# Optimization experiments

Hardware: AMD Instinct MI355X
Metric: run time of the kernel (lower is better)

Reference implementation:

```python
import jax, jax.numpy as jnp
import numpy as np
from jax import lax

K = 31          # mip_kernel
P_LO, P_HI = 0.01, 0.99
ALPHA = 0.15
MU = 10.0
PD_ITERS = 30
TAU = 0.125
SIG = 0.125
THETA = 1.0
EPS = 1e-6


def _max_pool(x, k):
    # torch F.max_pool2d with stride=1, padding=k//2 pads with -inf
    p = k // 2
    return lax.reduce_window(
        x, -jnp.inf, lax.max,
        window_dimensions=(1, 1, k, k),
        window_strides=(1, 1, 1, 1),
        padding=[(0, 0), (0, 0), (p, p), (p, p)])


def _forward_grad(u):
    # forward differences, zero-padded on the far edge (same shape as u)
    dx = jnp.pad(u[..., :, 1:] - u[..., :, :-1], ((0, 0), (0, 0), (0, 0), (0, 1)))
    dy = jnp.pad(u[..., 1:, :] - u[..., :-1, :], ((0, 0), (0, 0), (0, 1), (0, 0)))
    return dx, dy


def _divergence(px, py):
    div_x = px - jnp.pad(px[..., :, :-1], ((0, 0), (0, 0), (0, 0), (1, 0)))
    div_y = py - jnp.pad(py[..., :-1, :], ((0, 0), (0, 0), (1, 0), (0, 0)))
    return div_x + div_y


def _robust_normalize(x):
    B = x.shape[0]
    flat = x.reshape(B, -1)
    lo = jnp.quantile(flat, P_LO, axis=1).reshape(B, 1, 1, 1)
    hi = jnp.quantile(flat, P_HI, axis=1).reshape(B, 1, 1, 1)
    return jnp.clip((x - lo) / (hi - lo + EPS), 0.0, 1.0)


def setup_inputs() -> dict:
    key = jax.random.key(0)
    Iy = jax.random.uniform(key, (16, 3, 512, 512), dtype=jnp.float32)
    return {"Iy": Iy}


def reference(Iy):
    B = Iy.shape[0]
    R, G, Bc = Iy[:, 0:1], Iy[:, 1:2], Iy[:, 2:3]

    Rmax = _max_pool(R, K)
    GBmax = jnp.maximum(_max_pool(G, K), _max_pool(Bc, K))
    Dmip_abs = jnp.abs(Rmax - GBmax)

    N_hat = _robust_normalize(Dmip_abs + R)

    dxh, dyh = _forward_grad(N_hat)
    grad_mag = jnp.sqrt(dxh * dxh + dyh * dyh + EPS)
    # sigma_mode == 'median' -> per-image median of grad magnitude
    sigma = jnp.quantile(grad_mag.reshape(B, -1), 0.5, axis=1).reshape(B, 1, 1, 1)
    sigma = jnp.maximum(sigma, EPS)

    Wx = 1.0 + MU * jnp.exp(-jnp.abs(dxh) / sigma)
    Wy = 1.0 + MU * jnp.exp(-jnp.abs(dyh) / sigma)

    def step(carry, _):
        u, u_bar, px, py = carry
        dx, dy = _forward_grad(u_bar)
        px = jnp.clip(px + SIG * dx, -ALPHA * Wx, ALPHA * Wx)
        py = jnp.clip(py + SIG * dy, -ALPHA * Wy, ALPHA * Wy)
        div_p = _divergence(px, py)
        v = u + TAU * div_p
        u_new = (v + TAU * N_hat) / (1.0 + TAU)
        u_bar = u_new + THETA * (u_new - u)
        return (u_new, u_bar, px, py), None

    z = jnp.zeros_like(N_hat)
    (u, _, _, _), _ = lax.scan(step, (N_hat, N_hat, z, z), None, length=PD_ITERS)
    return jnp.clip(u, 0.0, 1.0)
```

## Files before the change

kernel.cpp:

```cpp
#include <hip/hip_runtime.h>
#include <hip/hip_bf16.h>
#include <hip/hip_fp16.h>
#include <math.h>

#define NPIX   262144
#define NP     4194304
#define NBINS  8192
#define HSUB   16
#define RB     8
#define SIG    0.125f
#define TAUC   0.125f
#define ALPHAC 0.15f
#define MUC    10.0f
#define EPSC   1e-6f
#define NEGINF -3.4e38f
#define IVT    (1.0f / (1.0f + TAUC))

__device__ __forceinline__ void cvt8h(float4 raw, float* d) {
    const __half2* h = (const __half2*)&raw;
#pragma unroll
    for (int j = 0; j < 4; ++j) {
        float2 f = __half22float2(h[j]);
        d[2 * j] = f.x; d[2 * j + 1] = f.y;
    }
}
__device__ __forceinline__ void ld8h(const __half* p, float* d) {
    cvt8h(*(const float4*)p, d);
}
__device__ __forceinline__ void ld8f(const float* p, float* d) {
    float4 t0 = *(const float4*)p;
    float4 t1 = *(const float4*)(p + 4);
    d[0]=t0.x; d[1]=t0.y; d[2]=t0.z; d[3]=t0.w;
    d[4]=t1.x; d[5]=t1.y; d[6]=t1.z; d[7]=t1.w;
}
__device__ __forceinline__ float4 pk8h(const float* s) {
    float4 r; __half2* h = (__half2*)&r;
#pragma unroll
    for (int j = 0; j < 4; ++j) h[j] = __floats2half2_rn(s[2 * j], s[2 * j + 1]);
    return r;
}
__device__ __forceinline__ float bnd(float d, float inv) {
    return ALPHAC * (1.f + MUC * __expf(-fabsf(d) * inv));
}
__device__ __forceinline__ float clmp(float v, float b) {
    return fminf(fmaxf(v, -b), b);
}


__global__ __launch_bounds__(512) void hpass3_k(const float* __restrict__ Iy,
                                                float* __restrict__ H) {
    __shared__ float rowbuf[8][512];
    __shared__ float PB[8][512];
    __shared__ float SB[8][512];
    int tid = threadIdx.x;
    int plane = blockIdx.y;
    int y0 = blockIdx.x * 8;

#pragma unroll
    for (int q = 0; q < 2; ++q) {
        int idx = q * 512 + tid;
        int r = idx >> 7;
        int x4 = (idx & 127) << 2;
        float4 v;
        if (plane < 16) {
            v = *(const float4*)(Iy + (size_t)(plane * 3) * NPIX + (size_t)(y0 + r) * 512 + x4);
        } else {
            int b = plane - 16;
            float4 g = *(const float4*)(Iy + ((size_t)(b * 3) + 1) * NPIX + (size_t)(y0 + r) * 512 + x4);
            float4 bb = *(const float4*)(Iy + ((size_t)(b * 3) + 2) * NPIX + (size_t)(y0 + r) * 512 + x4);
            v = make_float4(fmaxf(g.x, bb.x), fmaxf(g.y, bb.y), fmaxf(g.z, bb.z), fmaxf(g.w, bb.w));
        }
        *(float4*)(&rowbuf[r][x4]) = v;
    }
    __syncthreads();

    if (tid < 272) {
        int type = tid / 136;
        int rem = tid % 136;
        int r = rem / 17;
        int seg = rem % 17;
        int s0 = seg * 31;
        if (type == 0) {
            float run = rowbuf[r][s0];
            PB[r][s0] = run;
            for (int j = 1; j < 31; ++j) {
                int idx = s0 + j;
                if (idx < 512) { run = fmaxf(run, rowbuf[r][idx]); PB[r][idx] = run; }
            }
        } else {
            int s1 = min(s0 + 30, 511);
            float run = rowbuf[r][s1];
            SB[r][s1] = run;
            for (int j = s1 - 1; j >= s0; --j) { run = fmaxf(run, rowbuf[r][j]); SB[r][j] = run; }
        }
    }
    __syncthreads();

    int x = tid, a = x - 15, bc = x + 15;
#pragma unroll
    for (int r = 0; r < 8; ++r) {
        float o;
        if (a < 0)        o = PB[r][bc];
        else if (bc > 511) o = fmaxf(SB[r][a], PB[r][511]);
        else              o = fmaxf(SB[r][a], PB[r][bc]);
        H[(size_t)plane * NPIX + (size_t)(y0 + r) * 512 + x] = o;
    }
}

__global__ __launch_bounds__(64) void vpassC_k(const float* __restrict__ H,
                                               const float* __restrict__ Iy,
                                               float* __restrict__ xb) {
    int x = blockIdx.x * 64 + threadIdx.x;
    int b = blockIdx.z;
    const float* inR = H + (size_t)b * NPIX;
    const float* inM = H + (size_t)(16 + b) * NPIX;
    const float* IyR = Iy + (size_t)(b * 3) * NPIX;
    float*       out = xb + (size_t)b * NPIX;
    int c0 = blockIdx.y * 2;

    float SprevR[31], SprevM[31];
    if (c0 > 0) {
        int s0 = (c0 - 1) * 31;
        float vR[31], vM[31];
#pragma unroll
        for (int j = 0; j < 31; ++j) {
            vR[j] = inR[(size_t)(s0 + j) * 512 + x];
            vM[j] = inM[(size_t)(s0 + j) * 512 + x];
        }
        float aR = NEGINF, aM = NEGINF;
#pragma unroll
        for (int j = 30; j >= 0; --j) {
            aR = fmaxf(aR, vR[j]); SprevR[j] = aR;
            aM = fmaxf(aM, vM[j]); SprevM[j] = aM;
        }
    } else {
#pragma unroll
        for (int j = 0; j < 31; ++j) { SprevR[j] = NEGINF; SprevM[j] = NEGINF; }
    }

    int send = min(c0 + 1, 16);
    for (int s = c0; s <= send; ++s) {
        int s0 = s * 31;
        float vR[31], vM[31];
#pragma unroll
        for (int j = 0; j < 31; ++j) {
            bool ok = (s0 + j < 512);
            vR[j] = ok ? inR[(size_t)(s0 + j) * 512 + x] : NEGINF;
            vM[j] = ok ? inM[(size_t)(s0 + j) * 512 + x] : NEGINF;
        }
        float ScurR[31], ScurM[31];
        float aR = NEGINF, aM = NEGINF;
#pragma unroll
        for (int j = 30; j >= 0; --j) {
            aR = fmaxf(aR, vR[j]); ScurR[j] = aR;
            aM = fmaxf(aM, vM[j]); ScurM[j] = aM;
        }
        float PR = NEGINF, PM = NEGINF;
#pragma unroll
        for (int r = 0; r < 31; ++r) {
            PR = fmaxf(PR, vR[r]);
            PM = fmaxf(PM, vM[r]);
            int i = s0 + r - 15;
            if (i >= 0 && i <= 511) {
                int a = s0 - 30 + r;
                float oR, oM;
                if (a < 0) { oR = PR; oM = PM; }
                else {
                    float SvR = (r == 30) ? ScurR[0] : SprevR[r + 1];
                    float SvM = (r == 30) ? ScurM[0] : SprevM[r + 1];
                    oR = fmaxf(SvR, PR);
                    oM = fmaxf(SvM, PM);
                }
                out[(size_t)i * 512 + x] = fabsf(oR - oM) + IyR[(size_t)i * 512 + x];
            }
        }
#pragma unroll
        for (int j = 0; j < 31; ++j) { SprevR[j] = ScurR[j]; SprevM[j] = ScurM[j]; }
    }
}


__global__ __launch_bounds__(1024) void zeroi_k(int* __restrict__ p) {
    p[blockIdx.x * 1024 + threadIdx.x] = 0;
}

__global__ __launch_bounds__(1024) void hist2_k(const float* __restrict__ v,
                                                int* __restrict__ hist) {
    __shared__ int lh[NBINS];
    int s = blockIdx.x, b = blockIdx.y, tid = threadIdx.x;
    for (int i = tid; i < NBINS; i += 1024) lh[i] = 0;
    __syncthreads();
    const float* p = v + (size_t)b * NPIX + (size_t)s * (NPIX / HSUB);
    for (int i = tid; i < NPIX / HSUB; i += 1024) {
        int bin = (int)(p[i] * (NBINS * 0.5f));
        bin = min(max(bin, 0), NBINS - 1);
        atomicAdd(&lh[bin], 1);
    }
    __syncthreads();
    for (int i = tid; i < NBINS; i += 1024) {
        int c = lh[i];
        if (c) atomicAdd(&hist[b * NBINS + i], c);
    }
}

__global__ __launch_bounds__(1024) void gradhisth_k(const __half* __restrict__ nh,
                                                    int* __restrict__ hist) {
    __shared__ int lh[NBINS];
    int s = blockIdx.x, b = blockIdx.y, tid = threadIdx.x;
    for (int i = tid; i < NBINS; i += 1024) lh[i] = 0;
    __syncthreads();
    const __half* p = nh + (size_t)b * NPIX;
    int base = s * (NPIX / HSUB);
    for (int ii = tid; ii < NPIX / HSUB; ii += 1024) {
        int i = base + ii;
        float c = __half2float(p[i]);
        int x = i & 511, y = i >> 9;
        float dx = (x < 511) ? __half2float(p[i + 1])   - c : 0.f;
        float dy = (y < 511) ? __half2float(p[i + 512]) - c : 0.f;
        float gm = sqrtf(dx * dx + dy * dy + EPSC);
        int bin = (int)(gm * (NBINS * 0.5f));
        bin = min(max(bin, 0), NBINS - 1);
        atomicAdd(&lh[bin], 1);
    }
    __syncthreads();
    for (int i = tid; i < NBINS; i += 1024) {
        int c = lh[i];
        if (c) atomicAdd(&hist[b * NBINS + i], c);
    }
}

__global__ __launch_bounds__(1024) void quant2_k(const int* __restrict__ hist,
                                                 float* __restrict__ scal,
                                                 float q0, float q1, int s0, int s1) {
    __shared__ int csum[1025];
    __shared__ int wsum[16];
    int b = blockIdx.x, tid = threadIdx.x;
    const int* h = hist + b * NBINS;
    int s = 0;
#pragma unroll
    for (int j = 0; j < NBINS / 1024; ++j) s += h[tid * (NBINS / 1024) + j];

    int lane = tid & 63, wave = tid >> 6;
    int v = s;
#pragma unroll
    for (int off = 1; off < 64; off <<= 1) {
        int n = __shfl_up(v, off, 64);
        if (lane >= off) v += n;
    }
    if (lane == 63) wsum[wave] = v;
    __syncthreads();
    if (wave == 0 && lane < 16) {
        int w = wsum[lane];
#pragma unroll
        for (int off = 1; off < 16; off <<= 1) {
            int n = __shfl_up(w, off, 64);
            if (lane >= off) w += n;
        }
        wsum[lane] = w;
    }
    __syncthreads();
    int incl = v + (wave > 0 ? wsum[wave - 1] : 0);
    csum[tid + 1] = incl;
    if (tid == 0) csum[0] = 0;
    __syncthreads();

#pragma unroll
    for (int pass = 0; pass < 2; ++pass) {
        int slot = pass ? s1 : s0;
        if (slot < 0) continue;
        float q = pass ? q1 : q0;
        float t = q * (float)(NPIX - 1);
        if ((float)csum[tid] <= t && (float)csum[tid + 1] > t) {
            const int per = NBINS / 1024;
            int cb = csum[tid];
            int bin = tid * per;
            int hv = 1;
            for (int j = 0; j < per; ++j) {
                hv = h[tid * per + j];
                if ((float)(cb + hv) > t) { bin = tid * per + j; break; }
                cb += hv;
            }
            float k = t - (float)cb;
            scal[b * 4 + slot] = ((float)bin + (k + 0.5f) / (float)hv) * (2.0f / NBINS);
        }
    }
}

__global__ __launch_bounds__(256) void nhat2h_k(const float* __restrict__ xb,
                                                const float* __restrict__ scal,
                                                __half* __restrict__ nhh) {
    size_t i = ((size_t)blockIdx.x * 256 + threadIdx.x) * 4;
    int b = (int)(i >> 18);
    float lo = scal[b * 4 + 0], hi = scal[b * 4 + 1];
    float inv = 1.0f / (hi - lo + EPSC);
    float4 v = *(const float4*)(xb + i);
    float a0 = fminf(fmaxf((v.x - lo) * inv, 0.f), 1.f);
    float a1 = fminf(fmaxf((v.y - lo) * inv, 0.f), 1.f);
    float a2 = fminf(fmaxf((v.z - lo) * inv, 0.f), 1.f);
    float a3 = fminf(fmaxf((v.w - lo) * inv, 0.f), 1.f);
    *(__half2*)(nhh + i)     = __floats2half2_rn(a0, a1);
    *(__half2*)(nhh + i + 2) = __floats2half2_rn(a2, a3);
}

__global__ __launch_bounds__(256) void pdf2_k(const __half* __restrict__ u,
                                              const __half* __restrict__ up,
                                              const __half* __restrict__ pxO,
                                              const __half* __restrict__ pyO,
                                              __half* __restrict__ pxN,
                                              __half* __restrict__ pyN,
                                              const __half* __restrict__ nh,
                                              const float* __restrict__ scal,
                                              __half* __restrict__ u1g,
                                              __half* __restrict__ u2g,
                                              float* __restrict__ outF,
                                              int last) {
    __shared__ __align__(16) char smem[75776];
    float  (*ubar0)[512] = (float (*)[512])smem;
    __half (*u1l)[512]   = (__half(*)[512])smem;
    __half (*u0l)[512]   = (__half(*)[512])(smem + 10240);
    __half (*nhl)[512]   = (__half(*)[512])(smem + 24576);
    __half (*px1)[512]   = (__half(*)[512])(smem + 36864);
    __half (*py1)[512]   = (__half(*)[512])(smem + 47104);
    __half (*px2l)[512]  = (__half(*)[512])(smem + 58368);
    __half (*py2l)[512]  = (__half(*)[512])(smem + 66560);

    int tid = threadIdx.x;
    int sub = tid >> 6, lane = tid & 63, x0 = lane * 8;
    int y0 = blockIdx.x * RB;
    int b = blockIdx.y;
    size_t plane = (size_t)b * NPIX;
    float sgm = fmaxf(scal[b * 4 + 2], EPSC);
    float inv = 1.0f / sgm;
    const float4 z4 = make_float4(0.f, 0.f, 0.f, 0.f);

    for (int i = sub; i < 12; i += 4) {
        int g = y0 - 2 + i;
        if (g >= 0 && g < 512) {
            size_t off = plane + (size_t)g * 512 + x0;
            float uu[8], pp[8];
            ld8h(u + off, uu); ld8h(up + off, pp);
#pragma unroll
            for (int j = 0; j < 8; ++j) ubar0[i][x0 + j] = 2.f * uu[j] - pp[j];
            *(float4*)&nhl[i][x0] = *(const float4*)(nh + off);
        } else {
            *(float4*)&ubar0[i][x0]     = z4;
            *(float4*)&ubar0[i][x0 + 4] = z4;
            *(float4*)&nhl[i][x0] = z4;
        }
    }
    __syncthreads();

    for (int c = sub; c < 11; c += 4) {
        int g = y0 - 2 + c;
        if (g >= 0 && g < 512) {
            size_t off = plane + (size_t)g * 512 + x0;
            float nhc[8], nhd[8], ubc[8], ubd[8];
            ld8h(&nhl[c][x0], nhc);
            ld8h(&nhl[c + 1][x0], nhd);
            ld8f(&ubar0[c][x0], ubc);
            ld8f(&ubar0[c + 1][x0], ubd);
            float nhRr = (lane < 63) ? __half2float(nhl[c][x0 + 8]) : 0.f;
            float ubRr = (lane < 63) ? ubar0[c][x0 + 8] : 0.f;
            bool rD = (g < 511);
            float py0v[8]; ld8h(pyO + off, py0v);
            float pyv[8];
#pragma unroll
            for (int j = 0; j < 8; ++j) {
                float by = bnd(rD ? (nhd[j] - nhc[j]) : 0.f, inv);
                float dy = rD ? (ubd[j] - ubc[j]) : 0.f;
                pyv[j] = clmp(py0v[j] + SIG * dy, by);
            }
            *(float4*)&py1[c][x0] = pk8h(pyv);
            if (c >= 1) {
                float px0v[8]; ld8h(pxO + off, px0v);
                float pxv[8];
#pragma unroll
                for (int j = 0; j < 8; ++j) {
                    int x = x0 + j;
                    bool xok = (x < 511);
                    float nhr = (j < 7) ? nhc[j + 1] : nhRr;
                    float ubr = (j < 7) ? ubc[j + 1] : ubRr;
                    float bx = bnd(xok ? (nhr - nhc[j]) : 0.f, inv);
                    float dx = xok ? (ubr - ubc[j]) : 0.f;
                    pxv[j] = clmp(px0v[j] + SIG * dx, bx);
                }
                *(float4*)&px1[c - 1][x0] = pk8h(pxv);
            }
        } else {
            *(float4*)&py1[c][x0] = z4;
            if (c >= 1) *(float4*)&px1[c - 1][x0] = z4;
        }
    }
    __syncthreads();

    for (int a = sub; a < 10; a += 4) {
        int g = y0 - 1 + a;
        if (g >= 0 && g < 512) {
            size_t off = plane + (size_t)g * 512 + x0;
            float4 u0raw = *(const float4*)(u + off);
            float u0v[8]; cvt8h(u0raw, u0v);
            float nhc[8];  ld8h(&nhl[a + 1][x0], nhc);
            float px1c[8]; ld8h(&px1[a][x0], px1c);
            float py1c[8]; ld8h(&py1[a + 1][x0], py1c);
            float py1u[8]; ld8h(&py1[a][x0], py1u);
            float pxl = (x0 > 0) ? __half2float(px1[a][x0 - 1]) : 0.f;
            bool gU = (g > 0);
            float uv[8];
#pragma unroll
            for (int j = 0; j < 8; ++j) {
                int x = x0 + j;
                float left = (x > 0) ? ((j > 0) ? px1c[j - 1] : pxl) : 0.f;
                float div = px1c[j] - left + py1c[j] - (gU ? py1u[j] : 0.f);
                uv[j] = (u0v[j] + TAUC * div + TAUC * nhc[j]) * IVT;
            }
            float4 packed = pk8h(uv);
            *(float4*)&u1l[a][x0] = packed;
            *(float4*)&u0l[a][x0] = u0raw;
            if (g >= y0 && g < y0 + RB) *(float4*)(u1g + off) = packed;
        } else {
            *(float4*)&u1l[a][x0] = z4;
            *(float4*)&u0l[a][x0] = z4;
        }
    }
    __syncthreads();

    for (int e = sub; e < 9; e += 4) {
        int g = y0 - 1 + e;
        if (g >= 0) {
            size_t off = plane + (size_t)g * 512 + x0;
            float u1c[8], u0c[8], u1d[8], u0d[8];
            ld8h(&u1l[e][x0], u1c);     ld8h(&u0l[e][x0], u0c);
            ld8h(&u1l[e + 1][x0], u1d); ld8h(&u0l[e + 1][x0], u0d);
            float nhc[8], nhd[8];
            ld8h(&nhl[e + 1][x0], nhc); ld8h(&nhl[e + 2][x0], nhd);
            float ubc[8], ubd[8];
#pragma unroll
            for (int j = 0; j < 8; ++j) {
                ubc[j] = 2.f * u1c[j] - u0c[j];
                ubd[j] = 2.f * u1d[j] - u0d[j];
            }
            float ubRr = (lane < 63) ? (2.f * __half2float(u1l[e][x0 + 8]) - __half2float(u0l[e][x0 + 8])) : 0.f;
            float nhRr = (lane < 63) ? __half2float(nhl[e + 1][x0 + 8]) : 0.f;
            bool rD = (g < 511);
            float py1c[8]; ld8h(&py1[e + 1][x0], py1c);
            float pyv[8];
#pragma unroll
            for (int j = 0; j < 8; ++j) {
                float by = bnd(rD ? (nhd[j] - nhc[j]) : 0.f, inv);
                float dy = rD ? (ubd[j] - ubc[j]) : 0.f;
                pyv[j] = clmp(py1c[j] + SIG * dy, by);
            }
            float4 pyp = pk8h(pyv);
            *(float4*)&py2l[e][x0] = pyp;
            if (g >= y0) *(float4*)(pyN + off) = pyp;
            if (e >= 1) {
                float px1c[8]; ld8h(&px1[e][x0], px1c);
                float pxv[8];
#pragma unroll
                for (int j = 0; j < 8; ++j) {
                    int x = x0 + j;
                    bool xok = (x < 511);
                    float nhr = (j < 7) ? nhc[j + 1] : nhRr;
                    float ubr = (j < 7) ? ubc[j + 1] : ubRr;
                    float bx = bnd(xok ? (nhr - nhc[j]) : 0.f, inv);
                    float dx = xok ? (ubr - ubc[j]) : 0.f;
                    pxv[j] = clmp(px1c[j] + SIG * dx, bx);
                }
                float4 pxp = pk8h(pxv);
                *(float4*)&px2l[e - 1][x0] = pxp;
                *(float4*)(pxN + off) = pxp;
            }
        } else {
            *(float4*)&py2l[e][x0] = z4;
        }
    }
    __syncthreads();

    for (int d = sub; d < 8; d += 4) {
        int g = y0 + d;
        size_t off = plane + (size_t)g * 512 + x0;
        float px2c[8]; ld8h(&px2l[d][x0], px2c);
        float py2c[8]; ld8h(&py2l[d + 1][x0], py2c);
        float py2u[8]; ld8h(&py2l[d][x0], py2u);
        float pxl = (x0 > 0) ? __half2float(px2l[d][x0 - 1]) : 0.f;
        float u1c[8]; ld8h(&u1l[d + 1][x0], u1c);
        float nhc[8]; ld8h(&nhl[d + 2][x0], nhc);
        bool gU = (g > 0);
        float uv[8];
#pragma unroll
        for (int j = 0; j < 8; ++j) {
            int x = x0 + j;
            float left = (x > 0) ? ((j > 0) ? px2c[j - 1] : pxl) : 0.f;
            float div = px2c[j] - left + py2c[j] - (gU ? py2u[j] : 0.f);
            uv[j] = (u1c[j] + TAUC * div + TAUC * nhc[j]) * IVT;
        }
        if (last) {
            float4 o0, o1;
            o0.x = fminf(fmaxf(uv[0], 0.f), 1.f);
            o0.y = fminf(fmaxf(uv[1], 0.f), 1.f);
            o0.z = fminf(fmaxf(uv[2], 0.f), 1.f);
            o0.w = fminf(fmaxf(uv[3], 0.f), 1.f);
            o1.x = fminf(fmaxf(uv[4], 0.f), 1.f);
            o1.y = fminf(fmaxf(uv[5], 0.f), 1.f);
            o1.z = fminf(fmaxf(uv[6], 0.f), 1.f);
            o1.w = fminf(fmaxf(uv[7], 0.f), 1.f);
            *(float4*)(outF + off)     = o0;
            *(float4*)(outF + off + 4) = o1;
        } else {
            *(float4*)(u2g + off) = pk8h(uv);
        }
    }
}

extern "C" void kernel_launch(void* const* d_in, const int* in_sizes, int n_in,
                              void* d_out, int out_size, void* d_ws, size_t ws_size,
                              hipStream_t stream) {
    const float* Iy = (const float*)d_in[0];
    float* ws = (float*)d_ws;
    float* out = (float*)d_out;

    dim3 hist_g(HSUB, 16);
    dim3 pd2_g(512 / RB, 16);

    float*  xb = ws;
    float*  H  = ws + (size_t)NP;
    __half* hb = (__half*)(ws + (size_t)3 * NP);
    __half* nhh = hb;
    __half* HA  = hb + (size_t)NP;
    __half* HB  = hb + (size_t)2 * NP;
    __half* HC  = hb + (size_t)3 * NP;
    __half* HD  = hb + (size_t)4 * NP;
    __half* pxA = hb + (size_t)5 * NP;
    __half* pyA = hb + (size_t)6 * NP;
    __half* pxB = hb + (size_t)7 * NP;
    __half* pyB = hb + (size_t)8 * NP;
    int*    hist = (int*)(ws + (size_t)15 * NP / 2);
    float*  scal = ws + (size_t)15 * NP / 2 + 16 * NBINS;

    hpass3_k<<<dim3(64, 32), dim3(512), 0, stream>>>(Iy, H);
    vpassC_k<<<dim3(8, 9, 16), dim3(64), 0, stream>>>(H, Iy, xb);

    zeroi_k<<<16 * NBINS / 1024, 1024, 0, stream>>>(hist);
    hist2_k<<<hist_g, 1024, 0, stream>>>(xb, hist);
    quant2_k<<<16, 1024, 0, stream>>>(hist, scal, 0.01f, 0.99f, 0, 1);
    nhat2h_k<<<NP / 1024, 256, 0, stream>>>(xb, scal, nhh);

    zeroi_k<<<16 * NBINS / 1024, 1024, 0, stream>>>(hist);
    gradhisth_k<<<hist_g, 1024, 0, stream>>>(nhh, hist);
    quant2_k<<<16, 1024, 0, stream>>>(hist, scal, 0.5f, 0.5f, 2, -1);
    hipMemsetAsync(pxA, 0, (size_t)2 * NP * sizeof(__half), stream);

    const __half* ucur = nhh;
    const __half* uprev = nhh;
    __half* pxs[2] = {pxA, pxB};
    __half* pys[2] = {pyA, pyB};
    for (int k = 0; k < 15; ++k) {
        int cur = k & 1;
        __half* u1o = (k & 1) ? HC : HA;
        __half* u2o = (k & 1) ? HD : HB;
        pdf2_k<<<pd2_g, 256, 0, stream>>>(ucur, uprev,
                                          pxs[cur], pys[cur],
                                          pxs[cur ^ 1], pys[cur ^ 1],
                                          nhh, scal, u1o, u2o, out,
                                          (k == 14) ? 1 : 0);
        uprev = u1o;
        ucur = u2o;
    }
}
```

Measured before the change: 490.4 us.

## Shrink pdf2 LDS footprint by storing ubar in half and re-reading u/p from global

Cuts the fused two-iteration primal-dual kernel's shared memory from about 74KB to 46KB. It stores the initial ubar in fp16 instead of fp32 and drops the u0, px2 and py2 LDS tiles, re-reading u and the freshly written pxN/pyN from global memory (likely L2 hits). The u1 rows are stashed in registers so they can overwrite the aliased ubar region after an extra barrier. The aim is higher occupancy, at the cost of more global traffic, an extra sync, more registers and fp16 rounding of ubar.

```diff
diff --git a/kernel.cpp b/kernel.cpp
--- a/kernel.cpp
+++ b/kernel.cpp
@@ -26,12 +26,6 @@
 }
 __device__ __forceinline__ void ld8h(const __half* p, float* d) {
     cvt8h(*(const float4*)p, d);
-}
-__device__ __forceinline__ void ld8f(const float* p, float* d) {
-    float4 t0 = *(const float4*)p;
-    float4 t1 = *(const float4*)(p + 4);
-    d[0]=t0.x; d[1]=t0.y; d[2]=t0.z; d[3]=t0.w;
-    d[4]=t1.x; d[5]=t1.y; d[6]=t1.z; d[7]=t1.w;
 }
 __device__ __forceinline__ float4 pk8h(const float* s) {
     float4 r; __half2* h = (__half2*)&r;
@@ -314,15 +308,13 @@
                                               __half* __restrict__ u2g,
                                               float* __restrict__ outF,
                                               int last) {
-    __shared__ __align__(16) char smem[75776];
-    float  (*ubar0)[512] = (float (*)[512])smem;
-    __half (*u1l)[512]   = (__half(*)[512])smem;
-    __half (*u0l)[512]   = (__half(*)[512])(smem + 10240);
-    __half (*nhl)[512]   = (__half(*)[512])(smem + 24576);
-    __half (*px1)[512]   = (__half(*)[512])(smem + 36864);
-    __half (*py1)[512]   = (__half(*)[512])(smem + 47104);
-    __half (*px2l)[512]  = (__half(*)[512])(smem + 58368);
-    __half (*py2l)[512]  = (__half(*)[512])(smem + 66560);
+    __shared__ __align__(16) char smem[47104];
+    __half (*ubar0h)[512] = (__half(*)[512])smem;
+    __half (*u1l)[512]    = (__half(*)[512])smem;
+    __half (*nhl)[512]    = (__half(*)[512])(smem + 12288);
+    __half (*px1)[512]    = (__half(*)[512])(smem + 24576);
+    __half (*py1)[512]    = (__half(*)[512])(smem + 34816);
+    __half*  py2h         = (__half*)(smem + 46080);
 
     int tid = threadIdx.x;
     int sub = tid >> 6, lane = tid & 63, x0 = lane * 8;
@@ -337,14 +329,14 @@
         int g = y0 - 2 + i;
         if (g >= 0 && g < 512) {
             size_t off = plane + (size_t)g * 512 + x0;
-            float uu[8], pp[8];
+            float uu[8], pp[8], ub[8];
             ld8h(u + off, uu); ld8h(up + off, pp);
 #pragma unroll
-            for (int j = 0; j < 8; ++j) ubar0[i][x0 + j] = 2.f * uu[j] - pp[j];
+            for (int j = 0; j < 8; ++j) ub[j] = 2.f * uu[j] - pp[j];
+            *(float4*)&ubar0h[i][x0] = pk8h(ub);
             *(float4*)&nhl[i][x0] = *(const float4*)(nh + off);
         } else {
-            *(float4*)&ubar0[i][x0]     = z4;
-            *(float4*)&ubar0[i][x0 + 4] = z4;
+            *(float4*)&ubar0h[i][x0] = z4;
             *(float4*)&nhl[i][x0] = z4;
         }
     }
@@ -357,10 +349,10 @@
             float nhc[8], nhd[8], ubc[8], ubd[8];
             ld8h(&nhl[c][x0], nhc);
             ld8h(&nhl[c + 1][x0], nhd);
-            ld8f(&ubar0[c][x0], ubc);
-            ld8f(&ubar0[c + 1][x0], ubd);
+            ld8h(&ubar0h[c][x0], ubc);
+            ld8h(&ubar0h[c + 1][x0], ubd);
             float nhRr = (lane < 63) ? __half2float(nhl[c][x0 + 8]) : 0.f;
-            float ubRr = (lane < 63) ? ubar0[c][x0 + 8] : 0.f;
+            float ubRr = (lane < 63) ? __half2float(ubar0h[c][x0 + 8]) : 0.f;
             bool rD = (g < 511);
             float py0v[8]; ld8h(pyO + off, py0v);
             float pyv[8];
@@ -393,19 +385,20 @@
     }
     __syncthreads();
 
+    float u1stash[3][8];
+    int   u1rows = 0;
     for (int a = sub; a < 10; a += 4) {
         int g = y0 - 1 + a;
+        float uv[8];
         if (g >= 0 && g < 512) {
             size_t off = plane + (size_t)g * 512 + x0;
-            float4 u0raw = *(const float4*)(u + off);
-            float u0v[8]; cvt8h(u0raw, u0v);
+            float u0v[8]; ld8h(u + off, u0v);
             float nhc[8];  ld8h(&nhl[a + 1][x0], nhc);
             float px1c[8]; ld8h(&px1[a][x0], px1c);
             float py1c[8]; ld8h(&py1[a + 1][x0], py1c);
             float py1u[8]; ld8h(&py1[a][x0], py1u);
             float pxl = (x0 > 0) ? __half2float(px1[a][x0 - 1]) : 0.f;
             bool gU = (g > 0);
-            float uv[8];
 #pragma unroll
             for (int j = 0; j < 8; ++j) {
                 int x = x0 + j;
@@ -413,13 +406,25 @@
                 float div = px1c[j] - left + py1c[j] - (gU ? py1u[j] : 0.f);
                 uv[j] = (u0v[j] + TAUC * div + TAUC * nhc[j]) * IVT;
             }
-            float4 packed = pk8h(uv);
+        } else {
+#pragma unroll
+            for (int j = 0; j < 8; ++j) uv[j] = 0.f;
+        }
+#pragma unroll
+        for (int j = 0; j < 8; ++j) u1stash[u1rows][j] = uv[j];
+        ++u1rows;
+    }
+    __syncthreads();
+    {
+        int k = 0;
+        for (int a = sub; a < 10; a += 4, ++k) {
+            int g = y0 - 1 + a;
+            float4 packed = pk8h(u1stash[k]);
             *(float4*)&u1l[a][x0] = packed;
-            *(float4*)&u0l[a][x0] = u0raw;
-            if (g >= y0 && g < y0 + RB) *(float4*)(u1g + off) = packed;
-        } else {
-            *(float4*)&u1l[a][x0] = z4;
-            *(float4*)&u0l[a][x0] = z4;
+            if (g >= y0 && g < y0 + RB) {
+                size_t off = plane + (size_t)g * 512 + x0;
+                *(float4*)(u1g + off) = packed;
+            }
         }
     }
     __syncthreads();
@@ -428,20 +433,26 @@
         int g = y0 - 1 + e;
         if (g >= 0) {
             size_t off = plane + (size_t)g * 512 + x0;
-            float u1c[8], u0c[8], u1d[8], u0d[8];
-            ld8h(&u1l[e][x0], u1c);     ld8h(&u0l[e][x0], u0c);
-            ld8h(&u1l[e + 1][x0], u1d); ld8h(&u0l[e + 1][x0], u0d);
+            bool rD = (g < 511);
+            float u1c[8], u1d[8], u0c[8], u0d[8];
+            ld8h(&u1l[e][x0], u1c);
+            ld8h(&u1l[e + 1][x0], u1d);
+            ld8h(u + off, u0c);
+            if (rD) ld8h(u + off + 512, u0d);
+            else {
+#pragma unroll
+                for (int j = 0; j < 8; ++j) u0d[j] = 0.f;
+            }
             float nhc[8], nhd[8];
             ld8h(&nhl[e + 1][x0], nhc); ld8h(&nhl[e + 2][x0], nhd);
             float ubc[8], ubd[8];
 #pragma unroll
             for (int j = 0; j < 8; ++j) {
                 ubc[j] = 2.f * u1c[j] - u0c[j];
-                ubd[j] = 2.f * u1d[j] - u0d[j];
-            }
-            float ubRr = (lane < 63) ? (2.f * __half2float(u1l[e][x0 + 8]) - __half2float(u0l[e][x0 + 8])) : 0.f;
+                ubd[j] = rD ? (2.f * u1d[j] - u0d[j]) : 0.f;
+            }
+            float ubRr = (lane < 63) ? (2.f * __half2float(u1l[e][x0 + 8]) - __half2float(u[off + 8])) : 0.f;
             float nhRr = (lane < 63) ? __half2float(nhl[e + 1][x0 + 8]) : 0.f;
-            bool rD = (g < 511);
             float py1c[8]; ld8h(&py1[e + 1][x0], py1c);
             float pyv[8];
 #pragma unroll
@@ -451,8 +462,8 @@
                 pyv[j] = clmp(py1c[j] + SIG * dy, by);
             }
             float4 pyp = pk8h(pyv);
-            *(float4*)&py2l[e][x0] = pyp;
-            if (g >= y0) *(float4*)(pyN + off) = pyp;
+            if (e == 0) *(float4*)&py2h[x0] = pyp;
+            else        *(float4*)(pyN + off) = pyp;
             if (e >= 1) {
                 float px1c[8]; ld8h(&px1[e][x0], px1c);
                 float pxv[8];
@@ -466,12 +477,10 @@
                     float dx = xok ? (ubr - ubc[j]) : 0.f;
                     pxv[j] = clmp(px1c[j] + SIG * dx, bx);
                 }
-                float4 pxp = pk8h(pxv);
-                *(float4*)&px2l[e - 1][x0] = pxp;
-                *(float4*)(pxN + off) = pxp;
-            }
-        } else {
-            *(float4*)&py2l[e][x0] = z4;
+                *(float4*)(pxN + off) = pk8h(pxv);
+            }
+        } else {
+            *(float4*)&py2h[x0] = z4;
         }
     }
     __syncthreads();
@@ -479,10 +488,12 @@
     for (int d = sub; d < 8; d += 4) {
         int g = y0 + d;
         size_t off = plane + (size_t)g * 512 + x0;
-        float px2c[8]; ld8h(&px2l[d][x0], px2c);
-        float py2c[8]; ld8h(&py2l[d + 1][x0], py2c);
-        float py2u[8]; ld8h(&py2l[d][x0], py2u);
-        float pxl = (x0 > 0) ? __half2float(px2l[d][x0 - 1]) : 0.f;
+        float px2c[8]; ld8h(pxN + off, px2c);
+        float py2c[8]; ld8h(pyN + off, py2c);
+        float py2u[8];
+        if (d == 0) ld8h(&py2h[x0], py2u);
+        else        ld8h(pyN + off - 512, py2u);
+        float pxl = (x0 > 0) ? __half2float(*(pxN + off - 1)) : 0.f;
         float u1c[8]; ld8h(&u1l[d + 1][x0], u1c);
         float nhc[8]; ld8h(&nhl[d + 2][x0], nhc);
         bool gU = (g > 0);
```

Result: slower. 530.7 us (+8.2%).

## Store max-pool intermediates in fp16 and skip final-iteration dual writes

Applied to the files above, without the earlier changes.

The horizontal max-pool output and the pre-normalisation buffer are now stored as fp16 instead of fp32. This halves traffic through hpass, vpass, the histogram and the normalise kernels, and the normalise kernel now handles 8 elements per thread. The last primal-dual iteration no longer writes px, py or u1 to global memory, since nothing reads them afterwards. Histogram zeroing is switched to hipMemsetAsync. Storing the intermediates in fp16 adds rounding before the quantile and clamp steps.

```diff
diff --git a/kernel.cpp b/kernel.cpp
--- a/kernel.cpp
+++ b/kernel.cpp
@@ -27,12 +27,6 @@
 __device__ __forceinline__ void ld8h(const __half* p, float* d) {
     cvt8h(*(const float4*)p, d);
 }
-__device__ __forceinline__ void ld8f(const float* p, float* d) {
-    float4 t0 = *(const float4*)p;
-    float4 t1 = *(const float4*)(p + 4);
-    d[0]=t0.x; d[1]=t0.y; d[2]=t0.z; d[3]=t0.w;
-    d[4]=t1.x; d[5]=t1.y; d[6]=t1.z; d[7]=t1.w;
-}
 __device__ __forceinline__ float4 pk8h(const float* s) {
     float4 r; __half2* h = (__half2*)&r;
 #pragma unroll
@@ -48,7 +42,7 @@
 
 
 __global__ __launch_bounds__(512) void hpass3_k(const float* __restrict__ Iy,
-                                                float* __restrict__ H) {
+                                                __half* __restrict__ H) {
     __shared__ float rowbuf[8][512];
     __shared__ float PB[8][512];
     __shared__ float SB[8][512];
@@ -103,19 +97,19 @@
         if (a < 0)        o = PB[r][bc];
         else if (bc > 511) o = fmaxf(SB[r][a], PB[r][511]);
         else              o = fmaxf(SB[r][a], PB[r][bc]);
-        H[(size_t)plane * NPIX + (size_t)(y0 + r) * 512 + x] = o;
-    }
-}
-
-__global__ __launch_bounds__(64) void vpassC_k(const float* __restrict__ H,
+        H[(size_t)plane * NPIX + (size_t)(y0 + r) * 512 + x] = __float2half_rn(o);
+    }
+}
+
+__global__ __launch_bounds__(64) void vpassC_k(const __half* __restrict__ H,
                                                const float* __restrict__ Iy,
-                                               float* __restrict__ xb) {
+                                               __half* __restrict__ xb) {
     int x = blockIdx.x * 64 + threadIdx.x;
     int b = blockIdx.z;
-    const float* inR = H + (size_t)b * NPIX;
-    const float* inM = H + (size_t)(16 + b) * NPIX;
+    const __half* inR = H + (size_t)b * NPIX;
+    const __half* inM = H + (size_t)(16 + b) * NPIX;
     const float* IyR = Iy + (size_t)(b * 3) * NPIX;
-    float*       out = xb + (size_t)b * NPIX;
+    __half*      out = xb + (size_t)b * NPIX;
     int c0 = blockIdx.y * 2;
 
     float SprevR[31], SprevM[31];
@@ -124,8 +118,8 @@
         float vR[31], vM[31];
 #pragma unroll
         for (int j = 0; j < 31; ++j) {
-            vR[j] = inR[(size_t)(s0 + j) * 512 + x];
-            vM[j] = inM[(size_t)(s0 + j) * 512 + x];
+            vR[j] = __half2float(inR[(size_t)(s0 + j) * 512 + x]);
+            vM[j] = __half2float(inM[(size_t)(s0 + j) * 512 + x]);
         }
         float aR = NEGINF, aM = NEGINF;
 #pragma unroll
@@ -145,8 +139,8 @@
 #pragma unroll
         for (int j = 0; j < 31; ++j) {
             bool ok = (s0 + j < 512);
-            vR[j] = ok ? inR[(size_t)(s0 + j) * 512 + x] : NEGINF;
-            vM[j] = ok ? inM[(size_t)(s0 + j) * 512 + x] : NEGINF;
+            vR[j] = ok ? __half2float(inR[(size_t)(s0 + j) * 512 + x]) : NEGINF;
+            vM[j] = ok ? __half2float(inM[(size_t)(s0 + j) * 512 + x]) : NEGINF;
         }
         float ScurR[31], ScurM[31];
         float aR = NEGINF, aM = NEGINF;
@@ -171,7 +165,8 @@
                     oR = fmaxf(SvR, PR);
                     oM = fmaxf(SvM, PM);
                 }
-                out[(size_t)i * 512 + x] = fabsf(oR - oM) + IyR[(size_t)i * 512 + x];
+                out[(size_t)i * 512 + x] =
+                    __float2half_rn(fabsf(oR - oM) + IyR[(size_t)i * 512 + x]);
             }
         }
 #pragma unroll
@@ -180,19 +175,15 @@
 }
 
 
-__global__ __launch_bounds__(1024) void zeroi_k(int* __restrict__ p) {
-    p[blockIdx.x * 1024 + threadIdx.x] = 0;
-}
-
-__global__ __launch_bounds__(1024) void hist2_k(const float* __restrict__ v,
+__global__ __launch_bounds__(1024) void hist2_k(const __half* __restrict__ v,
                                                 int* __restrict__ hist) {
     __shared__ int lh[NBINS];
     int s = blockIdx.x, b = blockIdx.y, tid = threadIdx.x;
     for (int i = tid; i < NBINS; i += 1024) lh[i] = 0;
     __syncthreads();
-    const float* p = v + (size_t)b * NPIX + (size_t)s * (NPIX / HSUB);
+    const __half* p = v + (size_t)b * NPIX + (size_t)s * (NPIX / HSUB);
     for (int i = tid; i < NPIX / HSUB; i += 1024) {
-        int bin = (int)(p[i] * (NBINS * 0.5f));
+        int bin = (int)(__half2float(p[i]) * (NBINS * 0.5f));
         bin = min(max(bin, 0), NBINS - 1);
         atomicAdd(&lh[bin], 1);
     }
@@ -286,20 +277,19 @@
     }
 }
 
-__global__ __launch_bounds__(256) void nhat2h_k(const float* __restrict__ xb,
+__global__ __launch_bounds__(256) void nhat2h_k(const __half* __restrict__ xb,
                                                 const float* __restrict__ scal,
                                                 __half* __restrict__ nhh) {
-    size_t i = ((size_t)blockIdx.x * 256 + threadIdx.x) * 4;
+    size_t i = ((size_t)blockIdx.x * 256 + threadIdx.x) * 8;
     int b = (int)(i >> 18);
     float lo = scal[b * 4 + 0], hi = scal[b * 4 + 1];
     float inv = 1.0f / (hi - lo + EPSC);
-    float4 v = *(const float4*)(xb + i);
-    float a0 = fminf(fmaxf((v.x - lo) * inv, 0.f), 1.f);
-    float a1 = fminf(fmaxf((v.y - lo) * inv, 0.f), 1.f);
-    float a2 = fminf(fmaxf((v.z - lo) * inv, 0.f), 1.f);
-    float a3 = fminf(fmaxf((v.w - lo) * inv, 0.f), 1.f);
-    *(__half2*)(nhh + i)     = __floats2half2_rn(a0, a1);
-    *(__half2*)(nhh + i + 2) = __floats2half2_rn(a2, a3);
+    float v[8]; ld8h(xb + i, v);
+    float a[8];
+#pragma unroll
+    for (int j = 0; j < 8; ++j)
+        a[j] = fminf(fmaxf((v[j] - lo) * inv, 0.f), 1.f);
+    *(float4*)(nhh + i) = pk8h(a);
 }
 
 __global__ __launch_bounds__(256) void pdf2_k(const __half* __restrict__ u,
@@ -357,8 +347,17 @@
             float nhc[8], nhd[8], ubc[8], ubd[8];
             ld8h(&nhl[c][x0], nhc);
             ld8h(&nhl[c + 1][x0], nhd);
-            ld8f(&ubar0[c][x0], ubc);
-            ld8f(&ubar0[c + 1][x0], ubd);
+            float t0[8], t1[8];
+            float4 a0 = *(float4*)&ubar0[c][x0];
+            float4 a1 = *(float4*)&ubar0[c][x0 + 4];
+            t0[0]=a0.x; t0[1]=a0.y; t0[2]=a0.z; t0[3]=a0.w;
+            t0[4]=a1.x; t0[5]=a1.y; t0[6]=a1.z; t0[7]=a1.w;
+            float4 b0 = *(float4*)&ubar0[c + 1][x0];
+            float4 b1 = *(float4*)&ubar0[c + 1][x0 + 4];
+            t1[0]=b0.x; t1[1]=b0.y; t1[2]=b0.z; t1[3]=b0.w;
+            t1[4]=b1.x; t1[5]=b1.y; t1[6]=b1.z; t1[7]=b1.w;
+#pragma unroll
+            for (int j = 0; j < 8; ++j) { ubc[j] = t0[j]; ubd[j] = t1[j]; }
             float nhRr = (lane < 63) ? __half2float(nhl[c][x0 + 8]) : 0.f;
             float ubRr = (lane < 63) ? ubar0[c][x0 + 8] : 0.f;
             bool rD = (g < 511);
@@ -416,7 +415,7 @@
             float4 packed = pk8h(uv);
             *(float4*)&u1l[a][x0] = packed;
             *(float4*)&u0l[a][x0] = u0raw;
-            if (g >= y0 && g < y0 + RB) *(float4*)(u1g + off) = packed;
+            if (!last && g >= y0 && g < y0 + RB) *(float4*)(u1g + off) = packed;
         } else {
             *(float4*)&u1l[a][x0] = z4;
             *(float4*)&u0l[a][x0] = z4;
@@ -452,7 +451,7 @@
             }
             float4 pyp = pk8h(pyv);
             *(float4*)&py2l[e][x0] = pyp;
-            if (g >= y0) *(float4*)(pyN + off) = pyp;
+            if (!last && g >= y0) *(float4*)(pyN + off) = pyp;
             if (e >= 1) {
                 float px1c[8]; ld8h(&px1[e][x0], px1c);
                 float pxv[8];
@@ -468,7 +467,7 @@
                 }
                 float4 pxp = pk8h(pxv);
                 *(float4*)&px2l[e - 1][x0] = pxp;
-                *(float4*)(pxN + off) = pxp;
+                if (!last) *(float4*)(pxN + off) = pxp;
             }
         } else {
             *(float4*)&py2l[e][x0] = z4;
@@ -516,15 +515,12 @@
                               void* d_out, int out_size, void* d_ws, size_t ws_size,
                               hipStream_t stream) {
     const float* Iy = (const float*)d_in[0];
-    float* ws = (float*)d_ws;
     float* out = (float*)d_out;
 
     dim3 hist_g(HSUB, 16);
     dim3 pd2_g(512 / RB, 16);
 
-    float*  xb = ws;
-    float*  H  = ws + (size_t)NP;
-    __half* hb = (__half*)(ws + (size_t)3 * NP);
+    __half* hb  = (__half*)d_ws;
     __half* nhh = hb;
     __half* HA  = hb + (size_t)NP;
     __half* HB  = hb + (size_t)2 * NP;
@@ -534,18 +530,20 @@
     __half* pyA = hb + (size_t)6 * NP;
     __half* pxB = hb + (size_t)7 * NP;
     __half* pyB = hb + (size_t)8 * NP;
-    int*    hist = (int*)(ws + (size_t)15 * NP / 2);
-    float*  scal = ws + (size_t)15 * NP / 2 + 16 * NBINS;
-
-    hpass3_k<<<dim3(64, 32), dim3(512), 0, stream>>>(Iy, H);
-    vpassC_k<<<dim3(8, 9, 16), dim3(64), 0, stream>>>(H, Iy, xb);
-
-    zeroi_k<<<16 * NBINS / 1024, 1024, 0, stream>>>(hist);
-    hist2_k<<<hist_g, 1024, 0, stream>>>(xb, hist);
+    __half* xbh = hb + (size_t)9 * NP;
+    __half* Hh  = hb + (size_t)10 * NP;
+    int*    hist = (int*)(hb + (size_t)12 * NP);
+    float*  scal = (float*)(hist + 16 * NBINS);
+
+    hpass3_k<<<dim3(64, 32), dim3(512), 0, stream>>>(Iy, Hh);
+    vpassC_k<<<dim3(8, 9, 16), dim3(64), 0, stream>>>(Hh, Iy, xbh);
+
+    hipMemsetAsync(hist, 0, 16 * NBINS * sizeof(int), stream);
+    hist2_k<<<hist_g, 1024, 0, stream>>>(xbh, hist);
     quant2_k<<<16, 1024, 0, stream>>>(hist, scal, 0.01f, 0.99f, 0, 1);
-    nhat2h_k<<<NP / 1024, 256, 0, stream>>>(xb, scal, nhh);
-
-    zeroi_k<<<16 * NBINS / 1024, 1024, 0, stream>>>(hist);
+    nhat2h_k<<<NP / 2048, 256, 0, stream>>>(xbh, scal, nhh);
+
+    hipMemsetAsync(hist, 0, 16 * NBINS * sizeof(int), stream);
     gradhisth_k<<<hist_g, 1024, 0, stream>>>(nhh, hist);
     quant2_k<<<16, 1024, 0, stream>>>(hist, scal, 0.5f, 0.5f, 2, -1);
     hipMemsetAsync(pxA, 0, (size_t)2 * NP * sizeof(__half), stream);
```

Result: slower. 510.7 us (+4.1%).
